# Optimization experiments

Hardware: AMD Instinct MI355X
Metric: run time of the kernel (lower is better)

Reference implementation:

```python
import jax, jax.numpy as jnp
import numpy as np

N = 100000
E = 600000
IN_DIM = 128
OUT_DIM = 256
BN_EPS = 1e-5


def setup_inputs() -> dict:
    key = jax.random.key(0)
    ks = jax.random.split(key, 12)
    x = jax.random.normal(ks[0], (N, IN_DIM), dtype=jnp.float32)
    edge_index = jax.random.randint(ks[1], (2, E), 0, N, dtype=jnp.int64)
    s1 = 1.0 / np.sqrt(IN_DIM)
    s2 = 1.0 / np.sqrt(OUT_DIM)
    return {
        "x": x,
        "edge_index": edge_index,
        "eps": jnp.zeros((), dtype=jnp.float32),  # GINConv eps init = 0
        "W1": jax.random.uniform(ks[2], (IN_DIM, OUT_DIM), jnp.float32, -s1, s1),
        "b1": jnp.zeros((OUT_DIM,), jnp.float32),
        "W2": jax.random.uniform(ks[3], (OUT_DIM, OUT_DIM), jnp.float32, -s2, s2),
        "b2": jnp.zeros((OUT_DIM,), jnp.float32),
        "gamma": jnp.ones((OUT_DIM,), jnp.float32),
        "beta": jnp.zeros((OUT_DIM,), jnp.float32),
        "run_mean": jnp.zeros((OUT_DIM,), jnp.float32),
        "run_var": jnp.ones((OUT_DIM,), jnp.float32),
        "Wp": jax.random.uniform(ks[4], (IN_DIM, OUT_DIM), jnp.float32, -s1, s1),
        "bp": jnp.zeros((OUT_DIM,), jnp.float32),
    }


def reference(x, edge_index, eps, W1, b1, W2, b2, gamma, beta, run_mean, run_var, Wp, bp):
    src, dst = edge_index[0], edge_index[1]
    # GIN aggregation: sum_{j in N(i)} x_j  (scatter-add of source features to dst)
    agg = jax.ops.segment_sum(x[src], dst, num_segments=N)
    h = (1.0 + eps) * x + agg            # [N, in_dim]
    # 2-layer MLP (nn1)
    h = jax.nn.relu(h @ W1 + b1) @ W2 + b2   # [N, out_dim]
    # BatchNorm1d (eval mode: running stats); dropout = identity (eval)
    h = (h - run_mean) * jax.lax.rsqrt(run_var + BN_EPS) * gamma + beta
    # residual with projection (in_dim != out_dim)
    return h + x @ Wp + bp
```

## Files before the change

kernel.cpp:

```cpp
#include <hip/hip_runtime.h>

#define N_ 100000
#define E_ 600000
#define IND_ 128
#define OUTD_ 256
#define NT_ (N_/16)
#define NB_ 98
#define CASTN_ (N_*IND_/2)

typedef __attribute__((ext_vector_type(8))) short bf16x8;
typedef __attribute__((ext_vector_type(4))) float f32x4;
typedef __attribute__((ext_vector_type(2))) unsigned int u32x2;

static __device__ __forceinline__ unsigned f2bf_u(float f){
  union { float f; unsigned u; } v; v.f = f;
  return (v.u + 0x7fffu + ((v.u >> 16) & 1u)) >> 16;
}
static __device__ __forceinline__ unsigned pack2(float a, float b){
  return f2bf_u(a) | (f2bf_u(b) << 16);
}
static __device__ __forceinline__ float blo(unsigned u){
  union { unsigned u; float f; } v; v.u = u << 16; return v.f;
}
static __device__ __forceinline__ float bhi(unsigned u){
  union { unsigned u; float f; } v; v.u = u & 0xffff0000u; return v.f;
}
static __device__ __forceinline__ void gload_lds16(const bf16x8* g, bf16x8* l){
  __builtin_amdgcn_global_load_lds((const __attribute__((address_space(1))) void*)g,
                                   (__attribute__((address_space(3))) void*)l, 16, 0, 0);
}

__global__ void k_prep(const float* __restrict__ x,
                       const float* __restrict__ W1, const float* __restrict__ W2,
                       const float* __restrict__ Wp, const float* __restrict__ b2,
                       const float* __restrict__ gamma, const float* __restrict__ beta,
                       const float* __restrict__ mean, const float* __restrict__ var,
                       const float* __restrict__ bp,
                       const int* __restrict__ dst, int* __restrict__ deg,
                       unsigned short* __restrict__ W1s, unsigned short* __restrict__ W2s,
                       unsigned short* __restrict__ Wps,
                       float* __restrict__ scale, float* __restrict__ shift,
                       unsigned* __restrict__ xbw)
{
  int gid = blockIdx.x*256 + threadIdx.x;
  if (gid < 16384) {
    const float* W; unsigned short* Ws; int u;
    if (gid < 4096)       { W = W1; Ws = W1s; u = gid; }
    else if (gid < 12288) { W = W2; Ws = W2s; u = gid - 4096; }
    else                  { W = Wp; Ws = Wps; u = gid - 12288; }
    int l  = u & 63;
    int km = (u >> 6) & 1;
    int t  = (u >> 7) & 15;
    int q  = u >> 11;
    int kk = 2*q + km;
    int kb = kk*32 + (l >> 4)*8;
    int c  = 16*t + (l & 15);
    #pragma unroll
    for (int j = 0; j < 8; j++)
      Ws[u*8 + j] = (unsigned short)f2bf_u(W[(size_t)(kb + j)*OUTD_ + c]);
  } else if (gid < 16640) {
    int c = gid - 16384;
    float s = gamma[c] * rsqrtf(var[c] + 1e-5f);
    scale[c] = s;
    shift[c] = (b2[c] - mean[c]) * s + beta[c] + bp[c];
  } else if (gid < 16640 + CASTN_) {
    int ci = gid - 16640;
    float2 v = ((const float2*)x)[ci];
    xbw[ci] = pack2(v.x, v.y);
  } else if (gid < 16640 + CASTN_ + E_) {
    int e = gid - 16640 - CASTN_;
    atomicAdd(&deg[dst[e]], 1);
  }
}

__global__ __launch_bounds__(1024) void k_scan1(const int* __restrict__ deg,
                                                int* __restrict__ bsum, int* __restrict__ offs){
  __shared__ int red[16];
  int tid = threadIdx.x;
  int i = blockIdx.x*1024 + tid;
  int v = (i < N_) ? deg[i] : 0;
  #pragma unroll
  for (int d = 32; d; d >>= 1) v += __shfl_down(v, d);
  if ((tid & 63) == 0) red[tid >> 6] = v;
  __syncthreads();
  if (tid < 16) {
    int s = red[tid];
    #pragma unroll
    for (int d = 8; d; d >>= 1) s += __shfl_down(s, d, 16);
    if (tid == 0) bsum[blockIdx.x] = s;
  }
  if (blockIdx.x == 0 && tid == 0) offs[N_] = E_;
}

__global__ __launch_bounds__(1024) void k_scan2(const int* __restrict__ deg,
                                                const int* __restrict__ bsum, int* __restrict__ offs){
  __shared__ int bs[128];
  __shared__ int d1[1024];
  int tid = threadIdx.x;
  if (tid < 128) bs[tid] = (tid < NB_) ? bsum[tid] : 0;
  __syncthreads();
  #pragma unroll
  for (int d = 1; d < 128; d <<= 1){
    int v = (tid < 128 && tid >= d) ? bs[tid - d] : 0;
    __syncthreads();
    if (tid < 128) bs[tid] += v;
    __syncthreads();
  }
  int bprefix = (blockIdx.x > 0) ? bs[blockIdx.x - 1] : 0;
  int i = blockIdx.x*1024 + tid;
  int v = (i < N_) ? deg[i] : 0;
  d1[tid] = v;
  __syncthreads();
  #pragma unroll
  for (int d = 1; d < 1024; d <<= 1){
    int t = (tid >= d) ? d1[tid - d] : 0;
    __syncthreads();
    d1[tid] += t;
    __syncthreads();
  }
  if (i < N_) offs[i] = bprefix + d1[tid] - v;
}

__global__ void k_fill(const int* __restrict__ src, const int* __restrict__ dst,
                       const int* __restrict__ offs, int* __restrict__ cur, int* __restrict__ adj){
  int e = blockIdx.x*256 + threadIdx.x;
  if (e < E_) {
    int d = dst[e];
    int p = atomicAdd(&cur[d], 1);
    adj[offs[d] + p] = src[e];
  }
}

__global__ void k_agg(const unsigned* __restrict__ xb32, const int* __restrict__ offs,
                      const int* __restrict__ adj, const float* __restrict__ epsp,
                      unsigned* __restrict__ h0)
{
  int row  = blockIdx.x*4 + (threadIdx.x >> 6);
  int lane = threadIdx.x & 63;
  if (row >= N_) return;
  unsigned xw = xb32[(size_t)row*64 + lane];
  float ax0=0,ay0=0,ax1=0,ay1=0,ax2=0,ay2=0,ax3=0,ay3=0;
  float ax4=0,ay4=0,ax5=0,ay5=0,ax6=0,ay6=0,ax7=0,ay7=0;
  int b = offs[row], e = offs[row+1];
  for (int base = b; base < e; base += 64){
    int cnt = min(64, e - base);
    int idx = adj[base + min(lane, cnt - 1)];
    int j = 0;
    for (; j + 8 <= cnt; j += 8){
      int n0 = __shfl(idx, j+0), n1 = __shfl(idx, j+1);
      int n2 = __shfl(idx, j+2), n3 = __shfl(idx, j+3);
      int n4 = __shfl(idx, j+4), n5 = __shfl(idx, j+5);
      int n6 = __shfl(idx, j+6), n7 = __shfl(idx, j+7);
      unsigned v0 = xb32[(size_t)n0*64 + lane];
      unsigned v1 = xb32[(size_t)n1*64 + lane];
      unsigned v2 = xb32[(size_t)n2*64 + lane];
      unsigned v3 = xb32[(size_t)n3*64 + lane];
      unsigned v4 = xb32[(size_t)n4*64 + lane];
      unsigned v5 = xb32[(size_t)n5*64 + lane];
      unsigned v6 = xb32[(size_t)n6*64 + lane];
      unsigned v7 = xb32[(size_t)n7*64 + lane];
      ax0 += blo(v0); ay0 += bhi(v0);
      ax1 += blo(v1); ay1 += bhi(v1);
      ax2 += blo(v2); ay2 += bhi(v2);
      ax3 += blo(v3); ay3 += bhi(v3);
      ax4 += blo(v4); ay4 += bhi(v4);
      ax5 += blo(v5); ay5 += bhi(v5);
      ax6 += blo(v6); ay6 += bhi(v6);
      ax7 += blo(v7); ay7 += bhi(v7);
    }
    for (; j + 4 <= cnt; j += 4){
      int n0 = __shfl(idx, j+0), n1 = __shfl(idx, j+1);
      int n2 = __shfl(idx, j+2), n3 = __shfl(idx, j+3);
      unsigned v0 = xb32[(size_t)n0*64 + lane];
      unsigned v1 = xb32[(size_t)n1*64 + lane];
      unsigned v2 = xb32[(size_t)n2*64 + lane];
      unsigned v3 = xb32[(size_t)n3*64 + lane];
      ax0 += blo(v0); ay0 += bhi(v0);
      ax1 += blo(v1); ay1 += bhi(v1);
      ax2 += blo(v2); ay2 += bhi(v2);
      ax3 += blo(v3); ay3 += bhi(v3);
    }
    if (j + 2 <= cnt){
      int n0 = __shfl(idx, j+0), n1 = __shfl(idx, j+1);
      unsigned v0 = xb32[(size_t)n0*64 + lane];
      unsigned v1 = xb32[(size_t)n1*64 + lane];
      ax4 += blo(v0); ay4 += bhi(v0);
      ax5 += blo(v1); ay5 += bhi(v1);
      j += 2;
    }
    if (j < cnt){
      int n = __shfl(idx, j);
      unsigned v = xb32[(size_t)n*64 + lane];
      ax6 += blo(v); ay6 += bhi(v);
    }
  }
  float ax = ((ax0+ax1)+(ax2+ax3)) + ((ax4+ax5)+(ax6+ax7));
  float ay = ((ay0+ay1)+(ay2+ay3)) + ((ay4+ay5)+(ay6+ay7));
  float k1 = 1.f + epsp[0];
  h0[(size_t)row*64 + lane] = pack2(fmaf(k1, blo(xw), ax), fmaf(k1, bhi(xw), ay));
}

__global__ __launch_bounds__(256) void k_mlp(const unsigned short* __restrict__ h0,
        const unsigned short* __restrict__ xb16,
        const bf16x8* __restrict__ W1s, const float* __restrict__ b1,
        const bf16x8* __restrict__ W2s, const bf16x8* __restrict__ Wps,
        const float* __restrict__ scale, const float* __restrict__ shift,
        float* __restrict__ out)
{
  __shared__ bf16x8 w[2][2048];
  __shared__ __align__(16) char trans[4][2][1280];
  int tid = threadIdx.x;
  int wv = tid >> 6, lane = tid & 63, g = lane >> 4, r = lane & 15;
  int tile0 = blockIdx.x*4 + wv;
  int tile  = min(tile0, NT_ - 1);

  const bf16x8* hrow = (const bf16x8*)(h0 + ((size_t)tile*16 + r)*IND_);
  const bf16x8* xrow = (const bf16x8*)(xb16 + ((size_t)tile*16 + r)*IND_);
  bf16x8 B[4], XV[4];
  #pragma unroll
  for (int kk = 0; kk < 4; kk++) B[kk] = hrow[kk*4 + g];
  #pragma unroll
  for (int kk = 0; kk < 4; kk++) XV[kk] = xrow[kk*4 + g];

  auto STAGE = [&](int buf, const bf16x8* src){
    #pragma unroll
    for (int i = 0; i < 8; i++)
      gload_lds16(&src[i*256 + wv*64 + lane], &w[buf][i*256 + wv*64]);
  };
  f32x4 acc[16];
  auto MF = [&](int buf, bf16x8 f0, bf16x8 f1){
    #pragma unroll
    for (int t = 0; t < 16; t++)
      acc[t] = __builtin_amdgcn_mfma_f32_16x16x32_bf16(w[buf][(t*2+0)*64 + lane], f0, acc[t], 0,0,0);
    #pragma unroll
    for (int t = 0; t < 16; t++)
      acc[t] = __builtin_amdgcn_mfma_f32_16x16x32_bf16(w[buf][(t*2+1)*64 + lane], f1, acc[t], 0,0,0);
  };
  #pragma unroll
  for (int t = 0; t < 16; t++) acc[t] = (f32x4){0.f,0.f,0.f,0.f};

  STAGE(0, W1s);
  __syncthreads();

  STAGE(1, W1s + 2048);
  MF(0, B[0], B[1]);
  __syncthreads();

  STAGE(0, W2s);
  MF(1, B[2], B[3]);

  const float4* b1v = (const float4*)b1;
  bf16x8 H[8];
  #pragma unroll
  for (int kkh = 0; kkh < 8; kkh++){
    char* tr = &trans[wv][kkh & 1][0];
    #pragma unroll
    for (int h = 0; h < 2; h++){
      int t = 2*kkh + h;
      float4 bb = b1v[t*4 + g];
      f32x4 a = acc[t];
      float v0 = fmaxf(a.x + bb.x, 0.f);
      float v1 = fmaxf(a.y + bb.y, 0.f);
      float v2 = fmaxf(a.z + bb.z, 0.f);
      float v3 = fmaxf(a.w + bb.w, 0.f);
      u32x2 dd; dd.x = pack2(v0, v1); dd.y = pack2(v2, v3);
      *(u32x2*)(tr + r*80 + h*32 + g*8) = dd;
    }
    H[kkh] = *(const bf16x8*)(tr + r*80 + g*16);
  }
  #pragma unroll
  for (int t = 0; t < 16; t++) acc[t] = (f32x4){0.f,0.f,0.f,0.f};
  __syncthreads();

  STAGE(1, W2s + 2048);
  MF(0, H[0], H[1]);
  __syncthreads();

  STAGE(0, W2s + 4096);
  MF(1, H[2], H[3]);
  __syncthreads();

  STAGE(1, W2s + 6144);
  MF(0, H[4], H[5]);
  __syncthreads();

  STAGE(0, Wps);
  MF(1, H[6], H[7]);
  __syncthreads();

  STAGE(1, Wps + 2048);
  MF(0, XV[0], XV[1]);
  __syncthreads();

  MF(1, XV[2], XV[3]);

  if (tile0 < NT_){
    const float4* sc = (const float4*)scale;
    const float4* sh = (const float4*)shift;
    #pragma unroll
    for (int t = 0; t < 16; t++){
      float4 s = sc[t*4 + g], b = sh[t*4 + g];
      f32x4 a = acc[t];
      float4 o;
      o.x = fmaf(a.x, s.x, b.x);
      o.y = fmaf(a.y, s.y, b.y);
      o.z = fmaf(a.z, s.z, b.z);
      o.w = fmaf(a.w, s.w, b.w);
      *(float4*)(out + ((size_t)tile*16 + r)*OUTD_ + t*16 + g*4) = o;
    }
  }
}

extern "C" void kernel_launch(void* const* d_in, const int* in_sizes, int n_in,
                              void* d_out, int out_size, void* d_ws, size_t ws_size,
                              hipStream_t stream)
{
  const float* x     = (const float*)d_in[0];
  const int*   ei    = (const int*)d_in[1];
  const float* eps   = (const float*)d_in[2];
  const float* W1    = (const float*)d_in[3];
  const float* b1    = (const float*)d_in[4];
  const float* W2    = (const float*)d_in[5];
  const float* b2    = (const float*)d_in[6];
  const float* gamma = (const float*)d_in[7];
  const float* beta  = (const float*)d_in[8];
  const float* rmean = (const float*)d_in[9];
  const float* rvar  = (const float*)d_in[10];
  const float* Wp    = (const float*)d_in[11];
  const float* bp    = (const float*)d_in[12];
  float* out = (float*)d_out;

  char* ws = (char*)d_ws; size_t off = 0;
  auto carve = [&](size_t b)->char* { char* p = ws + off; off = (off + b + 255) & ~(size_t)255; return p; };
  unsigned*       xbuf  = (unsigned*)carve((size_t)CASTN_*4);
  unsigned*       h0    = (unsigned*)carve((size_t)N_*64*4);
  unsigned short* W1s   = (unsigned short*)carve(4096*16);
  unsigned short* W2s   = (unsigned short*)carve(8192*16);
  unsigned short* Wps   = (unsigned short*)carve(4096*16);
  float*          scale = (float*)carve(256*4);
  float*          shift = (float*)carve(256*4);
  int*            deg   = (int*)carve((size_t)N_*4);
  int*            cur   = (int*)carve((size_t)N_*4);
  int*            offs  = (int*)carve((size_t)(N_+1)*4);
  int*            adj   = (int*)carve((size_t)E_*4);
  int*            bsum  = (int*)carve((size_t)NB_*4);

  hipMemsetAsync(deg, 0, (size_t)N_*4, stream);
  hipMemsetAsync(cur, 0, (size_t)N_*4, stream);

  k_prep <<<(16640 + CASTN_ + E_ + 255)/256, 256, 0, stream>>>(x, W1, W2, Wp, b2, gamma, beta,
                                  rmean, rvar, bp, ei + E_, deg,
                                  W1s, W2s, Wps, scale, shift, xbuf);
  k_scan1<<<NB_, 1024, 0, stream>>>(deg, bsum, offs);
  k_scan2<<<NB_, 1024, 0, stream>>>(deg, bsum, offs);
  k_fill <<<(E_+255)/256, 256, 0, stream>>>(ei, ei + E_, offs, cur, adj);
  k_agg  <<<(N_+3)/4, 256, 0, stream>>>(xbuf, offs, adj, eps, h0);
  k_mlp  <<<(NT_+3)/4, 256, 0, stream>>>((const unsigned short*)h0, (const unsigned short*)xbuf,
                                         (const bf16x8*)W1s, b1, (const bf16x8*)W2s,
                                         (const bf16x8*)Wps, scale, shift, out);
}
```

Baseline: 186.5 us.

## Pipeline MLP weight staging through a 4-slot LDS ring with explicit vmcnt waits

Splits the weight staging into sixteen half-size slices held in a four-buffer LDS ring, prefetching two slices ahead. Each phase waits only on the vmcnt of its own slice before a barrier, and raises wave priority around the MFMA burst. The goal is to overlap global-to-LDS weight loads with matrix work and to avoid full __syncthreads drains. The cost is more barriers and hand-tuned vmcnt counts, which also assume the global loads issued earlier (B, XV) have already retired.

Measured after the change: 184.8 us. About the same (-0.9%).

```diff
diff --git a/kernel.cpp b/kernel.cpp
--- a/kernel.cpp
+++ b/kernel.cpp
@@ -207,7 +207,7 @@
         const float* __restrict__ scale, const float* __restrict__ shift,
         float* __restrict__ out)
 {
-  __shared__ bf16x8 w[2][2048];
+  __shared__ bf16x8 w[4][1024];
   __shared__ __align__(16) char trans[4][2][1280];
   int tid = threadIdx.x;
   int wv = tid >> 6, lane = tid & 63, g = lane >> 4, r = lane & 15;
@@ -222,32 +222,46 @@
   #pragma unroll
   for (int kk = 0; kk < 4; kk++) XV[kk] = xrow[kk*4 + g];
 
+  const bf16x8* sl[16];
+  #pragma unroll
+  for (int i = 0; i < 4; i++)  sl[i]      = W1s + i*1024;
+  #pragma unroll
+  for (int i = 0; i < 8; i++)  sl[4 + i]  = W2s + i*1024;
+  #pragma unroll
+  for (int i = 0; i < 4; i++)  sl[12 + i] = Wps + i*1024;
+
   auto STAGE = [&](int buf, const bf16x8* src){
     #pragma unroll
-    for (int i = 0; i < 8; i++)
+    for (int i = 0; i < 4; i++)
       gload_lds16(&src[i*256 + wv*64 + lane], &w[buf][i*256 + wv*64]);
   };
   f32x4 acc[16];
-  auto MF = [&](int buf, bf16x8 f0, bf16x8 f1){
-    #pragma unroll
-    for (int t = 0; t < 16; t++)
-      acc[t] = __builtin_amdgcn_mfma_f32_16x16x32_bf16(w[buf][(t*2+0)*64 + lane], f0, acc[t], 0,0,0);
-    #pragma unroll
-    for (int t = 0; t < 16; t++)
-      acc[t] = __builtin_amdgcn_mfma_f32_16x16x32_bf16(w[buf][(t*2+1)*64 + lane], f1, acc[t], 0,0,0);
+  auto MF16 = [&](int buf, bf16x8 f0, bf16x8 f1, int tb){
+    #pragma unroll
+    for (int tt = 0; tt < 8; tt++)
+      acc[tb+tt] = __builtin_amdgcn_mfma_f32_16x16x32_bf16(w[buf][(tt*2+0)*64 + lane], f0, acc[tb+tt], 0,0,0);
+    #pragma unroll
+    for (int tt = 0; tt < 8; tt++)
+      acc[tb+tt] = __builtin_amdgcn_mfma_f32_16x16x32_bf16(w[buf][(tt*2+1)*64 + lane], f1, acc[tb+tt], 0,0,0);
   };
   #pragma unroll
   for (int t = 0; t < 16; t++) acc[t] = (f32x4){0.f,0.f,0.f,0.f};
 
-  STAGE(0, W1s);
-  __syncthreads();
-
-  STAGE(1, W1s + 2048);
-  MF(0, B[0], B[1]);
-  __syncthreads();
-
-  STAGE(0, W2s);
-  MF(1, B[2], B[3]);
+#define PHASE(P, VM, F0, F1, TB)                                   \
+  { if ((P) + 2 < 16) STAGE(((P)+2)&3, sl[(P)+2]);                 \
+    asm volatile("s_waitcnt vmcnt(" VM ")" ::: "memory");          \
+    __builtin_amdgcn_s_barrier();                                  \
+    __builtin_amdgcn_s_setprio(1);                                 \
+    MF16((P)&3, F0, F1, TB);                                       \
+    __builtin_amdgcn_s_setprio(0); }
+
+  STAGE(0, sl[0]);
+  STAGE(1, sl[1]);
+
+  PHASE(0,  "8", B[0], B[1], 0)
+  PHASE(1,  "8", B[0], B[1], 8)
+  PHASE(2,  "8", B[2], B[3], 0)
+  PHASE(3,  "8", B[2], B[3], 8)
 
   const float4* b1v = (const float4*)b1;
   bf16x8 H[8];
@@ -270,29 +284,20 @@
   }
   #pragma unroll
   for (int t = 0; t < 16; t++) acc[t] = (f32x4){0.f,0.f,0.f,0.f};
-  __syncthreads();
-
-  STAGE(1, W2s + 2048);
-  MF(0, H[0], H[1]);
-  __syncthreads();
-
-  STAGE(0, W2s + 4096);
-  MF(1, H[2], H[3]);
-  __syncthreads();
-
-  STAGE(1, W2s + 6144);
-  MF(0, H[4], H[5]);
-  __syncthreads();
-
-  STAGE(0, Wps);
-  MF(1, H[6], H[7]);
-  __syncthreads();
-
-  STAGE(1, Wps + 2048);
-  MF(0, XV[0], XV[1]);
-  __syncthreads();
-
-  MF(1, XV[2], XV[3]);
+
+  PHASE(4,  "8", H[0], H[1], 0)
+  PHASE(5,  "8", H[0], H[1], 8)
+  PHASE(6,  "8", H[2], H[3], 0)
+  PHASE(7,  "8", H[2], H[3], 8)
+  PHASE(8,  "8", H[4], H[5], 0)
+  PHASE(9,  "8", H[4], H[5], 8)
+  PHASE(10, "8", H[6], H[7], 0)
+  PHASE(11, "8", H[6], H[7], 8)
+  PHASE(12, "8", XV[0], XV[1], 0)
+  PHASE(13, "8", XV[0], XV[1], 8)
+  PHASE(14, "4", XV[2], XV[3], 0)
+  PHASE(15, "0", XV[2], XV[3], 8)
+#undef PHASE
 
   if (tile0 < NT_){
     const float4* sc = (const float4*)scale;
```
